# Performance work log

Hardware: AMD Instinct MI355X
Metric: run time of the kernel (lower is better)

The kernel has to match this reference:

```python
import jax, jax.numpy as jnp
import numpy as np

VOCAB, EMB, UNITS, B, T = 50000, 300, 256, 32, 512


def _lstm_scan(x, Wi, Wh, b, h0, c0):
    """Keras-order LSTM (gates i,f,c,o). x: [B,T,D]. Returns (outputs [B,T,U], h, c)."""
    xg = jnp.einsum('btd,dg->btg', x, Wi) + b  # precompute input projections [B,T,4U]

    def step(carry, xt):
        h, c = carry
        g = xt + h @ Wh
        i, f, gg, o = jnp.split(g, 4, axis=-1)
        c = jax.nn.sigmoid(f) * c + jax.nn.sigmoid(i) * jnp.tanh(gg)
        h = jax.nn.sigmoid(o) * jnp.tanh(c)
        return (h, c), h

    (h, c), hs = jax.lax.scan(step, (h0, c0), jnp.swapaxes(xg, 0, 1))
    return jnp.swapaxes(hs, 0, 1), h, c


def _bilstm(x, pf, pb, init=None):
    """Keras Bidirectional(LSTM(go_backwards=True), merge_mode='sum').
    'forward' sub-layer scans reversed input; 'backward' sub-layer scans original
    input and its output is time-reversed before summing."""
    Bsz = x.shape[0]
    if init is None:
        z = jnp.zeros((Bsz, UNITS), x.dtype)
        hf0, cf0, hb0, cb0 = z, z, z, z
    else:
        hf0, cf0, hb0, cb0 = init
    of, hf, cf = _lstm_scan(x[:, ::-1], *pf, hf0, cf0)
    ob, hb, cb = _lstm_scan(x, *pb, hb0, cb0)
    return of + ob[:, ::-1], hf, cf, hb, cb


def setup_inputs() -> dict:
    key = jax.random.key(0)
    ks = iter(jax.random.split(key, 32))
    d = {}
    d['x'] = jax.random.randint(next(ks), (B, T), 0, VOCAB, dtype=jnp.int32)
    d['emb'] = jax.random.normal(next(ks), (VOCAB, EMB), jnp.float32) * 0.05
    dims_in = [EMB, UNITS, UNITS]
    for l in (1, 2, 3):
        for dirc in ('f', 'b'):
            din = dims_in[l - 1]
            d[f'Wi{l}{dirc}'] = jax.random.normal(next(ks), (din, 4 * UNITS), jnp.float32) * 0.05
            d[f'Wh{l}{dirc}'] = jax.random.normal(next(ks), (UNITS, 4 * UNITS), jnp.float32) * 0.05
            d[f'b{l}{dirc}'] = jnp.zeros((4 * UNITS,), jnp.float32)
    return d


def reference(x, emb, Wi1f, Wh1f, b1f, Wi1b, Wh1b, b1b,
              Wi2f, Wh2f, b2f, Wi2b, Wh2b, b2b,
              Wi3f, Wh3f, b3f, Wi3b, Wh3b, b3b):
    h = emb[x]  # embedding lookup [B,T,EMB]
    h, hf, cf, hb, cb = _bilstm(h, (Wi1f, Wh1f, b1f), (Wi1b, Wh1b, b1b))
    h, hf, cf, hb, cb = _bilstm(h, (Wi2f, Wh2f, b2f), (Wi2b, Wh2b, b2b), (hf, cf, hb, cb))
    out, hf, cf, hb, cb = _bilstm(h, (Wi3f, Wh3f, b3f), (Wi3b, Wh3b, b3b), (hf, cf, hb, cb))
    return out, hf, cf, hb, cb
```

## Files before the change

kernel.cpp:

```cpp
#include <hip/hip_runtime.h>
#include <stdint.h>


typedef unsigned short u16;
typedef __bf16 bf16x8 __attribute__((ext_vector_type(8)));
typedef float f32x4 __attribute__((ext_vector_type(4)));

#define SCOPE_AGENT __HIP_MEMORY_SCOPE_AGENT

__device__ __forceinline__ float bf2f(u16 u) { return __uint_as_float(((unsigned)u) << 16); }
__device__ __forceinline__ u16 f2bf(float f) {
  unsigned u = __float_as_uint(f);
  unsigned r = (u + 0x7FFFu + ((u >> 16) & 1u)) >> 16;
  return (u16)r;
}
__device__ __forceinline__ float rdW(const void* p, size_t i, int isf) {
  return isf ? ((const float*)p)[i] : bf2f(((const u16*)p)[i]);
}
__device__ __forceinline__ float sigf(float x) { return 1.f / (1.f + __expf(-x)); }
__device__ __forceinline__ float tanh_(float x) { float e = __expf(2.f * x); return 1.f - 2.f / (e + 1.f); }

#define O_X0   0ull
#define O_WC1  10485760ull
#define O_WC2  11796480ull
#define O_WC3  12845056ull
#define O_WH   13893632ull
#define O_BIAS 17039360ull
#define O_FLAG 17063936ull
#define O_CNT  17064000ull
#define O_C0   17076352ull
#define O_CA   17141888ull
#define O_CB   17207424ull
#define O_CC   17272960ull
#define O_HSA  17338496ull
#define O_HSB  34148480ull
#define O_XG   50958464ull

__global__ void k_detect(const unsigned* __restrict__ embw, unsigned* flag) {
  int tid = threadIdx.x;
  unsigned w = embw[tid];
  unsigned e = (w >> 7) & 0xFFu;
  unsigned long long m = __ballot(e >= 100u && e < 128u);
  if (tid == 0) flag[0] = (__popcll(m) >= 32) ? 0u : 1u;
}

__global__ __launch_bounds__(256) void k_prep(
    const void* Wi1f, const void* Wi1b, const void* Wi2f, const void* Wi2b,
    const void* Wi3f, const void* Wi3b,
    const void* Wh1f, const void* Wh1b, const void* Wh2f, const void* Wh2b,
    const void* Wh3f, const void* Wh3b,
    const void* b1f, const void* b1b, const void* b2f, const void* b2b,
    const void* b3f, const void* b3b,
    const unsigned* __restrict__ flag,
    u16* Wc1, u16* Wc2, u16* Wc3, u16* WhC, float* bias, unsigned* cnt, float* c0) {
  const int isf = (int)flag[0];
  int idx = blockIdx.x * 256 + threadIdx.x;
  if (idx < 2048 * 320) {
    int n = idx / 320, k = idx - n * 320;
    int dd = n >> 10, col = n & 1023;
    const void* W = dd ? Wi1b : Wi1f;
    Wc1[idx] = (k < 300) ? f2bf(rdW(W, (size_t)k * 1024 + col, isf)) : (u16)0;
  }
  if (idx < 2048 * 256) {
    int n = idx >> 8, k = idx & 255;
    int dd = n >> 10, col = n & 1023;
    Wc2[idx] = f2bf(rdW(dd ? Wi2b : Wi2f, (size_t)k * 1024 + col, isf));
    Wc3[idx] = f2bf(rdW(dd ? Wi3b : Wi3f, (size_t)k * 1024 + col, isf));
  }
  if (idx < 3 * 2048) {
    int l = idx >> 11, n = idx & 2047;
    int dd = n >> 10, col = n & 1023;
    const void* bp = (l == 0) ? (dd ? b1b : b1f) : (l == 1) ? (dd ? b2b : b2f) : (dd ? b3b : b3f);
    bias[idx] = rdW(bp, col, isf);
  }
  if (idx < 3 * 2 * 513) cnt[idx] = 0u;
  if (idx < 2 * 32 * 256) c0[idx] = 0.f;
  if (idx < 6 * 262144) {
    int mat = idx >> 18, pos = idx & 262143;
    const void* W = (mat == 0) ? Wh1f : (mat == 1) ? Wh1b : (mat == 2) ? Wh2f
                   : (mat == 3) ? Wh2b : (mat == 4) ? Wh3f : Wh3b;
    WhC[idx] = f2bf(rdW(W, (size_t)pos, isf));
  }
}

__global__ __launch_bounds__(256) void k_embed(const int* __restrict__ x,
                                               const void* __restrict__ emb,
                                               const unsigned* __restrict__ flag,
                                               u16* __restrict__ X0) {
  const int isf = (int)flag[0];
  int row = blockIdx.x;
  int t = row >> 5, b = row & 31;
  int tok = x[b * 512 + t];
  int tid = threadIdx.x;
  if (tid < 150) {
    unsigned pk;
    if (isf) {
      float2 v = *(const float2*)((const float*)emb + (size_t)tok * 300 + tid * 2);
      pk = (unsigned)f2bf(v.x) | ((unsigned)f2bf(v.y) << 16);
    } else {
      pk = *(const unsigned*)((const u16*)emb + (size_t)tok * 300 + tid * 2);
    }
    *(unsigned*)(X0 + (size_t)row * 320 + tid * 2) = pk;
  } else if (tid < 160) {
    *(unsigned*)(X0 + (size_t)row * 320 + 300 + (tid - 150) * 2) = 0u;
  }
}

__global__ __launch_bounds__(256) void k_gemm(const u16* __restrict__ A,
                                              const u16* __restrict__ Bt,
                                              const float* __restrict__ bias,
                                              u16* __restrict__ XG, int K) {
  __shared__ u16 As[128 * 32];
  __shared__ u16 Bs[128 * 32];
  const int tid = threadIdx.x;
  const int wv = tid >> 6, L = tid & 63, quad = L >> 4, l15 = L & 15;
  const int wm = wv & 1, wn = wv >> 1;
  const int bm = blockIdx.x & 127, bn = blockIdx.x >> 7;
  const u16* Ab = A + (size_t)(bm * 128) * K;
  const u16* Bb = Bt + (size_t)(bn * 128) * K;
  f32x4 z = {0.f, 0.f, 0.f, 0.f};
  f32x4 acc[4][4];
#pragma unroll
  for (int a = 0; a < 4; ++a)
#pragma unroll
    for (int b2 = 0; b2 < 4; ++b2) acc[a][b2] = z;
  const int srow = tid >> 2, sk = (tid & 3) * 8;
  for (int k0 = 0; k0 < K; k0 += 32) {
    __syncthreads();
    uint4 a0 = *(const uint4*)(Ab + (size_t)srow * K + k0 + sk);
    uint4 a1 = *(const uint4*)(Ab + (size_t)(srow + 64) * K + k0 + sk);
    uint4 b0 = *(const uint4*)(Bb + (size_t)srow * K + k0 + sk);
    uint4 b1 = *(const uint4*)(Bb + (size_t)(srow + 64) * K + k0 + sk);
    *(uint4*)&As[srow * 32 + sk] = a0;
    *(uint4*)&As[(srow + 64) * 32 + sk] = a1;
    *(uint4*)&Bs[srow * 32 + sk] = b0;
    *(uint4*)&Bs[(srow + 64) * 32 + sk] = b1;
    __syncthreads();
    bf16x8 af[4], bf[4];
#pragma unroll
    for (int t4 = 0; t4 < 4; ++t4) {
      af[t4] = *(const bf16x8*)&As[(wm * 64 + t4 * 16 + l15) * 32 + quad * 8];
      bf[t4] = *(const bf16x8*)&Bs[(wn * 64 + t4 * 16 + l15) * 32 + quad * 8];
    }
#pragma unroll
    for (int mt4 = 0; mt4 < 4; ++mt4)
#pragma unroll
      for (int nt4 = 0; nt4 < 4; ++nt4)
        acc[mt4][nt4] = __builtin_amdgcn_mfma_f32_16x16x32_bf16(af[mt4], bf[nt4], acc[mt4][nt4], 0, 0, 0);
  }
#pragma unroll
  for (int mt4 = 0; mt4 < 4; ++mt4)
#pragma unroll
    for (int nt4 = 0; nt4 < 4; ++nt4)
#pragma unroll
      for (int i = 0; i < 4; ++i) {
        int m = bm * 128 + wm * 64 + mt4 * 16 + quad * 4 + i;
        int n = bn * 128 + wn * 64 + nt4 * 16 + l15;
        XG[(size_t)m * 2048 + n] = f2bf(acc[mt4][nt4][i] + bias[n]);
      }
}

__global__ __launch_bounds__(256) void k_scan(const u16* __restrict__ XG,
                                              const u16* __restrict__ Whf,
                                              const u16* __restrict__ Whb,
                                              u16* hs, const u16* h0src,
                                              const float* __restrict__ c_src,
                                              float* __restrict__ c_dst,
                                              unsigned* cnt) {
  const int wg = blockIdx.x;
  const int d = wg >> 4, r = wg & 15;
  const int tid = threadIdx.x;
  const int wv = tid >> 6, L = tid & 63, quad = L >> 4, l15 = L & 15;
  const int mt = wv & 1, n0 = (wv >> 1) * 2;

  __shared__ u16 Ah[32][264];
  __shared__ float gbuf[32][68];

  const u16* Wh = d ? Whb : Whf;

  union U8 { u16 s[8]; bf16x8 v; };
  U8 bfrag[2][8];
#pragma unroll
  for (int nt2 = 0; nt2 < 2; ++nt2) {
    int gcol = (n0 + nt2) * 256 + r * 16 + l15;
#pragma unroll
    for (int kt = 0; kt < 8; ++kt)
#pragma unroll
      for (int j = 0; j < 8; ++j)
        bfrag[nt2][kt].s[j] = Wh[(size_t)(kt * 32 + quad * 8 + j) * 1024 + gcol];
  }

  const int b_c = tid >> 3, uu0 = tid & 7;
  float cv0 = c_src[(d * 32 + b_c) * 256 + r * 16 + uu0];
  float cv1 = c_src[(d * 32 + b_c) * 256 + r * 16 + uu0 + 8];

  {
    u16 v0 = 0, v1 = 0;
    if (h0src) {
      v0 = h0src[(size_t)(d * 513 + 512) * 8192 + b_c * 256 + r * 16 + uu0];
      v1 = h0src[(size_t)(d * 513 + 512) * 8192 + b_c * 256 + r * 16 + uu0 + 8];
    }
    hs[(size_t)(d * 513) * 8192 + b_c * 256 + r * 16 + uu0] = v0;
    hs[(size_t)(d * 513) * 8192 + b_c * 256 + r * 16 + uu0 + 8] = v1;
  }
  __syncthreads();
  if (tid == 0) __hip_atomic_fetch_add(&cnt[d * 513], 1u, __ATOMIC_RELEASE, SCOPE_AGENT);

  for (int s = 0; s < 512; ++s) {
    const int tin = d ? s : 511 - s;

    u16 xgr[2][4];
#pragma unroll
    for (int nt2 = 0; nt2 < 2; ++nt2) {
      int gcol = (n0 + nt2) * 256 + r * 16 + l15;
      const u16* xp = XG + (size_t)(tin * 32 + mt * 16 + quad * 4) * 2048 + d * 1024 + gcol;
#pragma unroll
      for (int i = 0; i < 4; ++i) xgr[nt2][i] = xp[(size_t)i * 2048];
    }

    if (tid == 0) {
      while (__hip_atomic_load(&cnt[d * 513 + s], __ATOMIC_ACQUIRE, SCOPE_AGENT) < 16u) {}
    }
    __syncthreads();

    {
      const u16* hp = hs + (size_t)(d * 513 + s) * 8192;
#pragma unroll
      for (int rep = 0; rep < 4; ++rep) {
        int pos = rep * 2048 + tid * 8;
        uint4 v = *(const uint4*)(hp + pos);
        *(uint4*)&Ah[pos >> 8][pos & 255] = v;
      }
    }
    __syncthreads();

    f32x4 acc0 = {0.f, 0.f, 0.f, 0.f}, acc1 = {0.f, 0.f, 0.f, 0.f};
#pragma unroll
    for (int kt = 0; kt < 8; ++kt) {
      bf16x8 ah = *(const bf16x8*)&Ah[mt * 16 + l15][kt * 32 + quad * 8];
      acc0 = __builtin_amdgcn_mfma_f32_16x16x32_bf16(ah, bfrag[0][kt].v, acc0, 0, 0, 0);
      acc1 = __builtin_amdgcn_mfma_f32_16x16x32_bf16(ah, bfrag[1][kt].v, acc1, 0, 0, 0);
    }

#pragma unroll
    for (int i = 0; i < 4; ++i) {
      int bb = mt * 16 + quad * 4 + i;
      gbuf[bb][(n0 + 0) * 16 + l15] = acc0[i] + bf2f(xgr[0][i]);
      gbuf[bb][(n0 + 1) * 16 + l15] = acc1[i] + bf2f(xgr[1][i]);
    }
    __syncthreads();

#pragma unroll
    for (int p = 0; p < 2; ++p) {
      int uu = uu0 + p * 8;
      float gi = gbuf[b_c][uu];
      float gf = gbuf[b_c][16 + uu];
      float gg = gbuf[b_c][32 + uu];
      float go = gbuf[b_c][48 + uu];
      float& c = p ? cv1 : cv0;
      c = sigf(gf) * c + sigf(gi) * tanh_(gg);
      float h = sigf(go) * tanh_(c);
      hs[(size_t)(d * 513 + s + 1) * 8192 + b_c * 256 + r * 16 + uu] = f2bf(h);
      if (s == 511) c_dst[(d * 32 + b_c) * 256 + r * 16 + uu] = c;
    }
    __syncthreads();
    if (tid == 0) __hip_atomic_fetch_add(&cnt[d * 513 + s + 1], 1u, __ATOMIC_RELEASE, SCOPE_AGENT);
  }
}

__global__ __launch_bounds__(256) void k_mkA(const u16* __restrict__ hs, u16* __restrict__ A23) {
  int row = blockIdx.x;
  int t = row >> 5, b = row & 31, u = threadIdx.x;
  float vf = bf2f(hs[(size_t)(t + 1) * 8192 + b * 256 + u]);
  float vb = bf2f(hs[(size_t)(513 + 512 - t) * 8192 + b * 256 + u]);
  A23[(size_t)row * 256 + u] = f2bf(vf + vb);
}

__global__ __launch_bounds__(256) void k_epi(const u16* __restrict__ hs,
                                             const float* __restrict__ cC,
                                             const unsigned* __restrict__ flag,
                                             void* __restrict__ outv) {
  const int isf = (int)flag[0];
  float* outf = (float*)outv;
  u16* outb = (u16*)outv;
  int u = threadIdx.x;
  if (blockIdx.x < 16384) {
    int b = blockIdx.x >> 9, s = blockIdx.x & 511;
    float v = bf2f(hs[(size_t)(s + 1) * 8192 + b * 256 + u]) +
              bf2f(hs[(size_t)(513 + 512 - s) * 8192 + b * 256 + u]);
    size_t o = (size_t)blockIdx.x * 256 + u;
    if (isf) outf[o] = v; else outb[o] = f2bf(v);
  } else {
    int j = blockIdx.x - 16384;
    const size_t base = 16384ull * 256;
    float vhf = bf2f(hs[(size_t)512 * 8192 + j * 256 + u]);
    float vcf = cC[j * 256 + u];
    float vhb = bf2f(hs[(size_t)1025 * 8192 + j * 256 + u]);
    float vcb = cC[(32 + j) * 256 + u];
    size_t o0 = base + (size_t)j * 256 + u;
    if (isf) {
      outf[o0] = vhf; outf[o0 + 8192] = vcf; outf[o0 + 16384] = vhb; outf[o0 + 24576] = vcb;
    } else {
      outb[o0] = f2bf(vhf); outb[o0 + 8192] = f2bf(vcf);
      outb[o0 + 16384] = f2bf(vhb); outb[o0 + 24576] = f2bf(vcb);
    }
  }
}

extern "C" void kernel_launch(void* const* d_in, const int* in_sizes, int n_in,
                              void* d_out, int out_size, void* d_ws, size_t ws_size,
                              hipStream_t stream) {
  (void)in_sizes; (void)n_in; (void)out_size; (void)ws_size;
  const int* x   = (const int*)d_in[0];
  const void* emb = d_in[1];
  const void* Wi1f = d_in[2];  const void* Wh1f = d_in[3];  const void* b1f = d_in[4];
  const void* Wi1b = d_in[5];  const void* Wh1b = d_in[6];  const void* b1b = d_in[7];
  const void* Wi2f = d_in[8];  const void* Wh2f = d_in[9];  const void* b2f = d_in[10];
  const void* Wi2b = d_in[11]; const void* Wh2b = d_in[12]; const void* b2b = d_in[13];
  const void* Wi3f = d_in[14]; const void* Wh3f = d_in[15]; const void* b3f = d_in[16];
  const void* Wi3b = d_in[17]; const void* Wh3b = d_in[18]; const void* b3b = d_in[19];

  char* ws = (char*)d_ws;
  u16* X0   = (u16*)(ws + O_X0);
  u16* A23  = (u16*)(ws + O_X0);
  u16* Wc1  = (u16*)(ws + O_WC1);
  u16* Wc2  = (u16*)(ws + O_WC2);
  u16* Wc3  = (u16*)(ws + O_WC3);
  u16* WhC  = (u16*)(ws + O_WH);
  float* bias = (float*)(ws + O_BIAS);
  unsigned* flag = (unsigned*)(ws + O_FLAG);
  unsigned* cnt = (unsigned*)(ws + O_CNT);
  float* c0 = (float*)(ws + O_C0);
  float* cA = (float*)(ws + O_CA);
  float* cB = (float*)(ws + O_CB);
  float* cC = (float*)(ws + O_CC);
  u16* hsA = (u16*)(ws + O_HSA);
  u16* hsB = (u16*)(ws + O_HSB);
  u16* XG  = (u16*)(ws + O_XG);

  k_detect<<<1, 64, 0, stream>>>((const unsigned*)emb, flag);
  k_prep<<<6144, 256, 0, stream>>>(Wi1f, Wi1b, Wi2f, Wi2b, Wi3f, Wi3b,
                                   Wh1f, Wh1b, Wh2f, Wh2b, Wh3f, Wh3b,
                                   b1f, b1b, b2f, b2b, b3f, b3b,
                                   flag, Wc1, Wc2, Wc3, WhC, bias, cnt, c0);
  k_embed<<<16384, 256, 0, stream>>>(x, emb, flag, X0);

  k_gemm<<<2048, 256, 0, stream>>>(X0, Wc1, bias + 0, XG, 320);
  k_scan<<<32, 256, 0, stream>>>(XG, WhC + 0 * 262144, WhC + 1 * 262144, hsA, nullptr, c0, cA, cnt);
  k_mkA<<<16384, 256, 0, stream>>>(hsA, A23);
  k_gemm<<<2048, 256, 0, stream>>>(A23, Wc2, bias + 2048, XG, 256);
  k_scan<<<32, 256, 0, stream>>>(XG, WhC + 2 * 262144, WhC + 3 * 262144, hsB, hsA, cA, cB, cnt + 1026);
  k_mkA<<<16384, 256, 0, stream>>>(hsB, A23);
  k_gemm<<<2048, 256, 0, stream>>>(A23, Wc3, bias + 4096, XG, 256);
  k_scan<<<32, 256, 0, stream>>>(XG, WhC + 4 * 262144, WhC + 5 * 262144, hsA, hsB, cB, cC, cnt + 2052);

  k_epi<<<16416, 256, 0, stream>>>(hsA, cC, flag, d_out);
}
```

Baseline: 4.726 ms.

## Replace counter barriers in LSTM scan with data-carried flags in hidden state

The recurrent scan drops the per-step atomic counter plus spin on a single thread. Each h word is now stored XOR-encoded so that a zero word means not yet written, and every thread polls its own slice of h until all words are non-zero. The grid is halved to 16 workgroups of 512 threads, each owning 32 units, and the next step's input projections are prefetched before the poll. In exchange, the hidden-state buffers must be zeroed before each scan and all readers of h must undo the XOR encoding.

```diff
diff --git a/kernel.cpp b/kernel.cpp
--- a/kernel.cpp
+++ b/kernel.cpp
@@ -27,7 +27,6 @@
 #define O_WH   13893632ull
 #define O_BIAS 17039360ull
 #define O_FLAG 17063936ull
-#define O_CNT  17064000ull
 #define O_C0   17076352ull
 #define O_CA   17141888ull
 #define O_CB   17207424ull
@@ -36,12 +35,20 @@
 #define O_HSB  34148480ull
 #define O_XG   50958464ull
 
+#define HS_U16 16809984ull
+#define HS_U4  1050624
+
 __global__ void k_detect(const unsigned* __restrict__ embw, unsigned* flag) {
   int tid = threadIdx.x;
   unsigned w = embw[tid];
   unsigned e = (w >> 7) & 0xFFu;
   unsigned long long m = __ballot(e >= 100u && e < 128u);
   if (tid == 0) flag[0] = (__popcll(m) >= 32) ? 0u : 1u;
+}
+
+__global__ __launch_bounds__(256) void k_zero(uint4* __restrict__ p, int n) {
+  uint4 z = {0u, 0u, 0u, 0u};
+  for (int i = blockIdx.x * 256 + threadIdx.x; i < n; i += gridDim.x * 256) p[i] = z;
 }
 
 __global__ __launch_bounds__(256) void k_prep(
@@ -52,7 +59,7 @@
     const void* b1f, const void* b1b, const void* b2f, const void* b2b,
     const void* b3f, const void* b3b,
     const unsigned* __restrict__ flag,
-    u16* Wc1, u16* Wc2, u16* Wc3, u16* WhC, float* bias, unsigned* cnt, float* c0) {
+    u16* Wc1, u16* Wc2, u16* Wc3, u16* WhC, float* bias, float* c0) {
   const int isf = (int)flag[0];
   int idx = blockIdx.x * 256 + threadIdx.x;
   if (idx < 2048 * 320) {
@@ -73,7 +80,6 @@
     const void* bp = (l == 0) ? (dd ? b1b : b1f) : (l == 1) ? (dd ? b2b : b2f) : (dd ? b3b : b3f);
     bias[idx] = rdW(bp, col, isf);
   }
-  if (idx < 3 * 2 * 513) cnt[idx] = 0u;
   if (idx < 2 * 32 * 256) c0[idx] = 0.f;
   if (idx < 6 * 262144) {
     int mat = idx >> 18, pos = idx & 262143;
@@ -160,78 +166,72 @@
       }
 }
 
-__global__ __launch_bounds__(256) void k_scan(const u16* __restrict__ XG,
+__global__ __launch_bounds__(512) void k_scan(const u16* __restrict__ XG,
                                               const u16* __restrict__ Whf,
                                               const u16* __restrict__ Whb,
                                               u16* hs, const u16* h0src,
                                               const float* __restrict__ c_src,
-                                              float* __restrict__ c_dst,
-                                              unsigned* cnt) {
+                                              float* __restrict__ c_dst) {
   const int wg = blockIdx.x;
-  const int d = wg >> 4, r = wg & 15;
+  const int d = wg >> 3, r = wg & 7;
   const int tid = threadIdx.x;
   const int wv = tid >> 6, L = tid & 63, quad = L >> 4, l15 = L & 15;
-  const int mt = wv & 1, n0 = (wv >> 1) * 2;
+  const int mt = wv & 1, p = wv >> 1;
 
   __shared__ u16 Ah[32][264];
-  __shared__ float gbuf[32][68];
+  __shared__ float gbuf[32][132];
 
   const u16* Wh = d ? Whb : Whf;
 
   union U8 { u16 s[8]; bf16x8 v; };
   U8 bfrag[2][8];
 #pragma unroll
-  for (int nt2 = 0; nt2 < 2; ++nt2) {
-    int gcol = (n0 + nt2) * 256 + r * 16 + l15;
+  for (int t = 0; t < 2; ++t) {
+    int nt = 2 * p + t;
+    int col = (nt >> 1) * 256 + r * 32 + (nt & 1) * 16 + l15;
 #pragma unroll
     for (int kt = 0; kt < 8; ++kt)
 #pragma unroll
       for (int j = 0; j < 8; ++j)
-        bfrag[nt2][kt].s[j] = Wh[(size_t)(kt * 32 + quad * 8 + j) * 1024 + gcol];
-  }
-
-  const int b_c = tid >> 3, uu0 = tid & 7;
-  float cv0 = c_src[(d * 32 + b_c) * 256 + r * 16 + uu0];
-  float cv1 = c_src[(d * 32 + b_c) * 256 + r * 16 + uu0 + 8];
+        bfrag[t][kt].s[j] = Wh[(size_t)(kt * 32 + quad * 8 + j) * 1024 + col];
+  }
+
+  const int b_c = tid >> 4, j16 = tid & 15;
+  const int gu = r * 32 + 2 * j16;
+  float cv0 = c_src[(d * 32 + b_c) * 256 + gu];
+  float cv1 = c_src[(d * 32 + b_c) * 256 + gu + 1];
+
+  unsigned* hw = (unsigned*)hs;
 
   {
-    u16 v0 = 0, v1 = 0;
+    unsigned hv[8];
     if (h0src) {
-      v0 = h0src[(size_t)(d * 513 + 512) * 8192 + b_c * 256 + r * 16 + uu0];
-      v1 = h0src[(size_t)(d * 513 + 512) * 8192 + b_c * 256 + r * 16 + uu0 + 8];
-    }
-    hs[(size_t)(d * 513) * 8192 + b_c * 256 + r * 16 + uu0] = v0;
-    hs[(size_t)(d * 513) * 8192 + b_c * 256 + r * 16 + uu0 + 8] = v1;
-  }
-  __syncthreads();
-  if (tid == 0) __hip_atomic_fetch_add(&cnt[d * 513], 1u, __ATOMIC_RELEASE, SCOPE_AGENT);
+      const unsigned* h0w = (const unsigned*)h0src + (size_t)(d * 513 + 512) * 4096 + tid * 8;
+#pragma unroll
+      for (int q = 0; q < 8; ++q) hv[q] = h0w[q];
+    } else {
+#pragma unroll
+      for (int q = 0; q < 8; ++q) hv[q] = 0x80008000u;
+    }
+    unsigned* dst = (unsigned*)&Ah[tid >> 4][(tid & 15) * 16];
+#pragma unroll
+    for (int q = 0; q < 8; ++q) dst[q] = hv[q] ^ 0x80008000u;
+  }
+
+  u16 xgr[2][4];
+  {
+    int tin = d ? 0 : 511;
+#pragma unroll
+    for (int t = 0; t < 2; ++t) {
+      int nt = 2 * p + t;
+      int col = d * 1024 + (nt >> 1) * 256 + r * 32 + (nt & 1) * 16 + l15;
+      const u16* xp = XG + (size_t)(tin * 32 + mt * 16 + quad * 4) * 2048 + col;
+#pragma unroll
+      for (int i = 0; i < 4; ++i) xgr[t][i] = xp[(size_t)i * 2048];
+    }
+  }
 
   for (int s = 0; s < 512; ++s) {
-    const int tin = d ? s : 511 - s;
-
-    u16 xgr[2][4];
-#pragma unroll
-    for (int nt2 = 0; nt2 < 2; ++nt2) {
-      int gcol = (n0 + nt2) * 256 + r * 16 + l15;
-      const u16* xp = XG + (size_t)(tin * 32 + mt * 16 + quad * 4) * 2048 + d * 1024 + gcol;
-#pragma unroll
-      for (int i = 0; i < 4; ++i) xgr[nt2][i] = xp[(size_t)i * 2048];
-    }
-
-    if (tid == 0) {
-      while (__hip_atomic_load(&cnt[d * 513 + s], __ATOMIC_ACQUIRE, SCOPE_AGENT) < 16u) {}
-    }
-    __syncthreads();
-
-    {
-      const u16* hp = hs + (size_t)(d * 513 + s) * 8192;
-#pragma unroll
-      for (int rep = 0; rep < 4; ++rep) {
-        int pos = rep * 2048 + tid * 8;
-        uint4 v = *(const uint4*)(hp + pos);
-        *(uint4*)&Ah[pos >> 8][pos & 255] = v;
-      }
-    }
     __syncthreads();
 
     f32x4 acc0 = {0.f, 0.f, 0.f, 0.f}, acc1 = {0.f, 0.f, 0.f, 0.f};
@@ -245,34 +245,85 @@
 #pragma unroll
     for (int i = 0; i < 4; ++i) {
       int bb = mt * 16 + quad * 4 + i;
-      gbuf[bb][(n0 + 0) * 16 + l15] = acc0[i] + bf2f(xgr[0][i]);
-      gbuf[bb][(n0 + 1) * 16 + l15] = acc1[i] + bf2f(xgr[1][i]);
+      {
+        int nt = 2 * p;
+        gbuf[bb][(nt >> 1) * 32 + (nt & 1) * 16 + l15] = acc0[i] + bf2f(xgr[0][i]);
+      }
+      {
+        int nt = 2 * p + 1;
+        gbuf[bb][(nt >> 1) * 32 + (nt & 1) * 16 + l15] = acc1[i] + bf2f(xgr[1][i]);
+      }
     }
     __syncthreads();
 
-#pragma unroll
-    for (int p = 0; p < 2; ++p) {
-      int uu = uu0 + p * 8;
-      float gi = gbuf[b_c][uu];
-      float gf = gbuf[b_c][16 + uu];
-      float gg = gbuf[b_c][32 + uu];
-      float go = gbuf[b_c][48 + uu];
-      float& c = p ? cv1 : cv0;
-      c = sigf(gf) * c + sigf(gi) * tanh_(gg);
-      float h = sigf(go) * tanh_(c);
-      hs[(size_t)(d * 513 + s + 1) * 8192 + b_c * 256 + r * 16 + uu] = f2bf(h);
-      if (s == 511) c_dst[(d * 32 + b_c) * 256 + r * 16 + uu] = c;
-    }
-    __syncthreads();
-    if (tid == 0) __hip_atomic_fetch_add(&cnt[d * 513 + s + 1], 1u, __ATOMIC_RELEASE, SCOPE_AGENT);
+    {
+      int lu = 2 * j16;
+      float gi0 = gbuf[b_c][lu],      gi1 = gbuf[b_c][lu + 1];
+      float gf0 = gbuf[b_c][32 + lu], gf1 = gbuf[b_c][32 + lu + 1];
+      float gg0 = gbuf[b_c][64 + lu], gg1 = gbuf[b_c][64 + lu + 1];
+      float go0 = gbuf[b_c][96 + lu], go1 = gbuf[b_c][96 + lu + 1];
+      cv0 = sigf(gf0) * cv0 + sigf(gi0) * tanh_(gg0);
+      cv1 = sigf(gf1) * cv1 + sigf(gi1) * tanh_(gg1);
+      float h0f = sigf(go0) * tanh_(cv0);
+      float h1f = sigf(go1) * tanh_(cv1);
+      u16 e0 = f2bf(h0f); if (e0 == 0x8000u) e0 = 0;
+      u16 e1 = f2bf(h1f); if (e1 == 0x8000u) e1 = 0;
+      unsigned pk = ((unsigned)e0 | ((unsigned)e1 << 16)) ^ 0x80008000u;
+      __hip_atomic_store(&hw[(size_t)(d * 513 + s + 1) * 4096 + b_c * 128 + r * 16 + j16],
+                         pk, __ATOMIC_RELAXED, SCOPE_AGENT);
+      if (s == 511) {
+        c_dst[(d * 32 + b_c) * 256 + gu] = cv0;
+        c_dst[(d * 32 + b_c) * 256 + gu + 1] = cv1;
+      }
+    }
+
+    if (s < 511) {
+      __syncthreads();
+
+      {
+        int tin = d ? (s + 1) : (510 - s);
+#pragma unroll
+        for (int t = 0; t < 2; ++t) {
+          int nt = 2 * p + t;
+          int col = d * 1024 + (nt >> 1) * 256 + r * 32 + (nt & 1) * 16 + l15;
+          const u16* xp = XG + (size_t)(tin * 32 + mt * 16 + quad * 4) * 2048 + col;
+#pragma unroll
+          for (int i = 0; i < 4; ++i) xgr[t][i] = xp[(size_t)i * 2048];
+        }
+      }
+
+      const unsigned long long* src =
+          (const unsigned long long*)(hw + (size_t)(d * 513 + s + 1) * 4096) + tid * 4;
+      unsigned long long w[4];
+#pragma unroll
+      for (int q2 = 0; q2 < 4; ++q2)
+        w[q2] = __hip_atomic_load(src + q2, __ATOMIC_RELAXED, SCOPE_AGENT);
+      for (;;) {
+        bool all = true;
+#pragma unroll
+        for (int q2 = 0; q2 < 4; ++q2) {
+          if ((unsigned)w[q2] == 0u || (unsigned)(w[q2] >> 32) == 0u) {
+            all = false;
+            w[q2] = __hip_atomic_load(src + q2, __ATOMIC_RELAXED, SCOPE_AGENT);
+          }
+        }
+        if (all) break;
+      }
+      unsigned* dst = (unsigned*)&Ah[tid >> 4][(tid & 15) * 16];
+#pragma unroll
+      for (int q2 = 0; q2 < 4; ++q2) {
+        dst[q2 * 2]     = ((unsigned)w[q2]) ^ 0x80008000u;
+        dst[q2 * 2 + 1] = ((unsigned)(w[q2] >> 32)) ^ 0x80008000u;
+      }
+    }
   }
 }
 
 __global__ __launch_bounds__(256) void k_mkA(const u16* __restrict__ hs, u16* __restrict__ A23) {
   int row = blockIdx.x;
   int t = row >> 5, b = row & 31, u = threadIdx.x;
-  float vf = bf2f(hs[(size_t)(t + 1) * 8192 + b * 256 + u]);
-  float vb = bf2f(hs[(size_t)(513 + 512 - t) * 8192 + b * 256 + u]);
+  float vf = bf2f(hs[(size_t)(t + 1) * 8192 + b * 256 + u] ^ 0x8000u);
+  float vb = bf2f(hs[(size_t)(513 + 512 - t) * 8192 + b * 256 + u] ^ 0x8000u);
   A23[(size_t)row * 256 + u] = f2bf(vf + vb);
 }
 
@@ -286,16 +337,16 @@
   int u = threadIdx.x;
   if (blockIdx.x < 16384) {
     int b = blockIdx.x >> 9, s = blockIdx.x & 511;
-    float v = bf2f(hs[(size_t)(s + 1) * 8192 + b * 256 + u]) +
-              bf2f(hs[(size_t)(513 + 512 - s) * 8192 + b * 256 + u]);
+    float v = bf2f(hs[(size_t)(s + 1) * 8192 + b * 256 + u] ^ 0x8000u) +
+              bf2f(hs[(size_t)(513 + 512 - s) * 8192 + b * 256 + u] ^ 0x8000u);
     size_t o = (size_t)blockIdx.x * 256 + u;
     if (isf) outf[o] = v; else outb[o] = f2bf(v);
   } else {
     int j = blockIdx.x - 16384;
     const size_t base = 16384ull * 256;
-    float vhf = bf2f(hs[(size_t)512 * 8192 + j * 256 + u]);
+    float vhf = bf2f(hs[(size_t)512 * 8192 + j * 256 + u] ^ 0x8000u);
     float vcf = cC[j * 256 + u];
-    float vhb = bf2f(hs[(size_t)1025 * 8192 + j * 256 + u]);
+    float vhb = bf2f(hs[(size_t)1025 * 8192 + j * 256 + u] ^ 0x8000u);
     float vcb = cC[(32 + j) * 256 + u];
     size_t o0 = base + (size_t)j * 256 + u;
     if (isf) {
@@ -329,7 +380,6 @@
   u16* WhC  = (u16*)(ws + O_WH);
   float* bias = (float*)(ws + O_BIAS);
   unsigned* flag = (unsigned*)(ws + O_FLAG);
-  unsigned* cnt = (unsigned*)(ws + O_CNT);
   float* c0 = (float*)(ws + O_C0);
   float* cA = (float*)(ws + O_CA);
   float* cB = (float*)(ws + O_CB);
@@ -342,17 +392,20 @@
   k_prep<<<6144, 256, 0, stream>>>(Wi1f, Wi1b, Wi2f, Wi2b, Wi3f, Wi3b,
                                    Wh1f, Wh1b, Wh2f, Wh2b, Wh3f, Wh3b,
                                    b1f, b1b, b2f, b2b, b3f, b3b,
-                                   flag, Wc1, Wc2, Wc3, WhC, bias, cnt, c0);
+                                   flag, Wc1, Wc2, Wc3, WhC, bias, c0);
+  k_zero<<<2048, 256, 0, stream>>>((uint4*)hsA, HS_U4);
+  k_zero<<<2048, 256, 0, stream>>>((uint4*)hsB, HS_U4);
   k_embed<<<16384, 256, 0, stream>>>(x, emb, flag, X0);
 
   k_gemm<<<2048, 256, 0, stream>>>(X0, Wc1, bias + 0, XG, 320);
-  k_scan<<<32, 256, 0, stream>>>(XG, WhC + 0 * 262144, WhC + 1 * 262144, hsA, nullptr, c0, cA, cnt);
+  k_scan<<<16, 512, 0, stream>>>(XG, WhC + 0 * 262144, WhC + 1 * 262144, hsA, nullptr, c0, cA);
   k_mkA<<<16384, 256, 0, stream>>>(hsA, A23);
   k_gemm<<<2048, 256, 0, stream>>>(A23, Wc2, bias + 2048, XG, 256);
-  k_scan<<<32, 256, 0, stream>>>(XG, WhC + 2 * 262144, WhC + 3 * 262144, hsB, hsA, cA, cB, cnt + 1026);
+  k_scan<<<16, 512, 0, stream>>>(XG, WhC + 2 * 262144, WhC + 3 * 262144, hsB, hsA, cA, cB);
+  k_zero<<<2048, 256, 0, stream>>>((uint4*)hsA, HS_U4);
   k_mkA<<<16384, 256, 0, stream>>>(hsB, A23);
   k_gemm<<<2048, 256, 0, stream>>>(A23, Wc3, bias + 4096, XG, 256);
-  k_scan<<<32, 256, 0, stream>>>(XG, WhC + 4 * 262144, WhC + 5 * 262144, hsA, hsB, cB, cC, cnt + 2052);
+  k_scan<<<16, 512, 0, stream>>>(XG, WhC + 4 * 262144, WhC + 5 * 262144, hsA, hsB, cB, cC);
 
   k_epi<<<16416, 256, 0, stream>>>(hsA, cC, flag, d_out);
 }
```

Result: faster. 4.014 ms (-15.1%).
